# Optimization experiments

Measured on AMD Instinct MI355X. Metric: run time of the kernel, lower is better.

## Reference

```python
import jax, jax.numpy as jnp
import numpy as np

B, S, F_, D, H, L, OUT = 2, 1024, 240, 512, 6, 6, 512
NH = 16
DH = D // NH
EPS = 1e-6  # fast_transformers causal-linear eps
LN_EPS = 1e-5  # torch LayerNorm default


def layernorm(x, g, b):
    m = x.mean(-1, keepdims=True)
    v = ((x - m) ** 2).mean(-1, keepdims=True)
    return (x - m) * jax.lax.rsqrt(v + LN_EPS) * g + b


def causal_linear_attn(q, k, v):
    # q,k,v: [B,S,NH,DH]; feature map phi(x)=elu(x)+1 (fast_transformers default)
    Q = jax.nn.elu(q) + 1.0
    K = jax.nn.elu(k) + 1.0
    # running sum of outer products K_i V_i^T -> [B,S,NH,DH,DH]
    kv = jnp.cumsum(jnp.einsum('bshd,bshm->bshdm', K, v), axis=1)
    num = jnp.einsum('bshd,bshdm->bshm', Q, kv)
    Z = 1.0 / (jnp.einsum('bshd,bshd->bsh', Q, jnp.cumsum(K, axis=1)) + EPS)
    return num * Z[..., None]


def setup_inputs() -> dict:
    key = jax.random.key(0)
    ks = iter(jax.random.split(key, 16))

    def w(shape, s=0.02):
        return (s * jax.random.normal(next(ks), shape)).astype(jnp.float32)

    f32 = jnp.float32
    return {
        'x': jax.random.normal(next(ks), (B, S, F_), dtype=f32),
        'g_in': jnp.ones((F_,), f32), 'b_in': jnp.zeros((F_,), f32),
        'W_pre': w((F_, D)), 'b_pre': jnp.zeros((D,), f32),
        'Wq': w((L, D, D)), 'bq': jnp.zeros((L, D), f32),
        'Wk': w((L, D, D)), 'bk': jnp.zeros((L, D), f32),
        'Wv': w((L, D, D)), 'bv': jnp.zeros((L, D), f32),
        'Wo': w((L, D, D)), 'bo': jnp.zeros((L, D), f32),
        'W1': w((L, D, D)), 'bf1': jnp.zeros((L, D), f32),  # feed_forward_dimensions == hidden_sz
        'W2': w((L, D, D)), 'bf2': jnp.zeros((L, D), f32),
        'ln1_g': jnp.ones((L, D), f32), 'ln1_b': jnp.zeros((L, D), f32),
        'ln2_g': jnp.ones((L, D), f32), 'ln2_b': jnp.zeros((L, D), f32),
        'lnf_g': jnp.ones((D,), f32), 'lnf_b': jnp.zeros((D,), f32),
        'W_post': w((D, OUT)), 'b_post': jnp.zeros((OUT,), f32),
    }


def reference(x, g_in, b_in, W_pre, b_pre, Wq, bq, Wk, bk, Wv, bv, Wo, bo,
              W1, bf1, W2, bf2, ln1_g, ln1_b, ln2_g, ln2_b, lnf_g, lnf_b,
              W_post, b_post):
    # input norm + pre projection
    h = layernorm(x, g_in, b_in) @ W_pre + b_pre  # [B,S,D]
    # fast_transformers post-norm encoder layers
    for l in range(L):
        q = (h @ Wq[l] + bq[l]).reshape(B, S, NH, DH)
        k = (h @ Wk[l] + bk[l]).reshape(B, S, NH, DH)
        v = (h @ Wv[l] + bv[l]).reshape(B, S, NH, DH)
        a = causal_linear_attn(q, k, v).reshape(B, S, D) @ Wo[l] + bo[l]
        h = layernorm(h + a, ln1_g[l], ln1_b[l])
        y = jax.nn.relu(h @ W1[l] + bf1[l]) @ W2[l] + bf2[l]
        h = layernorm(h + y, ln2_g[l], ln2_b[l])
    # final encoder norm, then post projection
    h = layernorm(h, lnf_g, lnf_b)
    return h @ W_post + b_post
```

## Files before the change

kernel.cpp:

```cpp
#include <hip/hip_runtime.h>
#include <hip/hip_bf16.h>
#include <cmath>

#define NROW 2048
#define DMODEL 512
#define FIN 240
#define FINPAD 256
#define NHEAD 16
#define DHEAD 32
#define CHUNK 64
#define NCHUNK 16
#define NLAYER 6
#define SEQ 1024
#define QKVLD 1536

typedef __attribute__((ext_vector_type(8))) short bf16x8;
typedef __attribute__((ext_vector_type(4))) float f32x4;
typedef __attribute__((ext_vector_type(4))) unsigned short u16x4;

#define MFMA_BF16 __builtin_amdgcn_mfma_f32_16x16x32_bf16

__device__ __forceinline__ float phi(float x) {
    return x > 0.f ? x + 1.f : expf(x);
}

__device__ __forceinline__ float bf2f(unsigned short u) {
    return __uint_as_float((unsigned)u << 16);
}

__device__ __forceinline__ unsigned short f2bf_bits(float z) {
    __hip_bfloat16 hb_ = __float2bfloat16(z);
    return *reinterpret_cast<unsigned short*>(&hb_);
}

__device__ __forceinline__ void load_lds16(const void* g, void* l) {
    __builtin_amdgcn_global_load_lds(
        (const __attribute__((address_space(1))) void*)g,
        (__attribute__((address_space(3))) void*)l, 16, 0, 0);
}

__global__ __launch_bounds__(64) void ln_kernel(
    const float* __restrict__ in, const float* __restrict__ res,
    const float* __restrict__ g, const float* __restrict__ b,
    float* __restrict__ out, __hip_bfloat16* __restrict__ outb,
    int C, int Cpad) {
    int row = blockIdx.x;
    int t = threadIdx.x;
    const float* xr = in + (size_t)row * C;
    const float* rr = res ? res + (size_t)row * C : nullptr;
    f32x4 v[2] = {{0.f,0.f,0.f,0.f},{0.f,0.f,0.f,0.f}};
    float sum = 0.f, sq = 0.f;
#pragma unroll
    for (int i = 0; i < 2; ++i) {
        int c = (t + i * 64) * 4;
        if (c < C) {
            f32x4 x_ = *(const f32x4*)&xr[c];
            if (rr) x_ += *(const f32x4*)&rr[c];
            v[i] = x_;
#pragma unroll
            for (int j = 0; j < 4; ++j) { sum += x_[j]; sq += x_[j] * x_[j]; }
        }
    }
#pragma unroll
    for (int off = 32; off > 0; off >>= 1) {
        sum += __shfl_xor(sum, off, 64);
        sq  += __shfl_xor(sq,  off, 64);
    }
    float mean = sum / (float)C;
    float var  = sq / (float)C - mean * mean;
    float rstd = rsqrtf(var + 1e-5f);
#pragma unroll
    for (int i = 0; i < 2; ++i) {
        int c = (t + i * 64) * 4;
        f32x4 y;
#pragma unroll
        for (int j = 0; j < 4; ++j) y[j] = (v[i][j] - mean) * rstd;
        if (c < C) {
            f32x4 gg = *(const f32x4*)&g[c];
            f32x4 bb = *(const f32x4*)&b[c];
#pragma unroll
            for (int j = 0; j < 4; ++j) y[j] = y[j] * gg[j] + bb[j];
            if (out) *(f32x4*)&out[(size_t)row * C + c] = y;
        }
        if (outb && c < Cpad) {
            u16x4 o;
#pragma unroll
            for (int j = 0; j < 4; ++j) {
                float z = (c + j < C) ? y[j] : 0.f;
                o[j] = f2bf_bits(z);
            }
            *(u16x4*)&outb[(size_t)row * Cpad + c] = o;
        }
    }
}

template<int RELU, int WF32, int WBF16, int PHI, int K>
__global__ __launch_bounds__(256) void gemm_bf16_kernel(
    const __hip_bfloat16* __restrict__ A, const __hip_bfloat16* __restrict__ Bt,
    const float* __restrict__ bias,
    float* __restrict__ C, __hip_bfloat16* __restrict__ Cb,
    int N) {
    constexpr int NSTEP = K / 64;
    __shared__ __align__(16) __hip_bfloat16 As[4][64][64];
    __shared__ __align__(16) __hip_bfloat16 Bs[4][64][64];
    const int tid = threadIdx.x, lane = tid & 63, w = tid >> 6;
    const int nN = N >> 6;
    const int bm = (blockIdx.x / nN) * 64;
    const int bn = (blockIdx.x % nN) * 64;

    const int srow  = lane >> 3;
    const int sslot = (lane & 7) ^ srow;
    const size_t aoff = (size_t)srow * K + (size_t)sslot * 8;
    const __hip_bfloat16* gA0 = A  + (size_t)(bm + w * 8) * K + aoff;
    const __hip_bfloat16* gA1 = A  + (size_t)(bm + 32 + w * 8) * K + aoff;
    const __hip_bfloat16* gB0 = Bt + (size_t)(bn + w * 8) * K + aoff;
    const __hip_bfloat16* gB1 = Bt + (size_t)(bn + 32 + w * 8) * K + aoff;

#define STAGE(t) do { \
        load_lds16(gA0 + (size_t)(t) * 64, &As[(t) & 3][w * 8][0]); \
        load_lds16(gA1 + (size_t)(t) * 64, &As[(t) & 3][32 + w * 8][0]); \
        load_lds16(gB0 + (size_t)(t) * 64, &Bs[(t) & 3][w * 8][0]); \
        load_lds16(gB1 + (size_t)(t) * 64, &Bs[(t) & 3][32 + w * 8][0]); \
    } while (0)

    const int wm = (w >> 1) << 5, wn = (w & 1) << 5;
    const int fr = lane & 15, fq = lane >> 4;
    const int sw = fr & 7;
    const int e0 = ((fq      ^ sw) << 3);
    const int e1 = (((fq | 4) ^ sw) << 3);
    f32x4 acc00 = {0.f, 0.f, 0.f, 0.f}, acc01 = acc00, acc10 = acc00, acc11 = acc00;

    STAGE(0); STAGE(1); STAGE(2);
#pragma unroll
    for (int t = 0; t < NSTEP; ++t) {
        if (NSTEP - t >= 3)      asm volatile("s_waitcnt vmcnt(8)" ::: "memory");
        else if (NSTEP - t == 2) asm volatile("s_waitcnt vmcnt(4)" ::: "memory");
        else                     asm volatile("s_waitcnt vmcnt(0)" ::: "memory");
        __builtin_amdgcn_s_barrier();
        __builtin_amdgcn_sched_barrier(0);
        if (t + 3 < NSTEP) STAGE(t + 3);
        const int b = t & 3;
        bf16x8 a00 = *(const bf16x8*)&As[b][wm + fr][e0];
        bf16x8 a01 = *(const bf16x8*)&As[b][wm + fr][e1];
        bf16x8 a10 = *(const bf16x8*)&As[b][wm + 16 + fr][e0];
        bf16x8 a11 = *(const bf16x8*)&As[b][wm + 16 + fr][e1];
        bf16x8 b00 = *(const bf16x8*)&Bs[b][wn + fr][e0];
        bf16x8 b01 = *(const bf16x8*)&Bs[b][wn + fr][e1];
        bf16x8 b10 = *(const bf16x8*)&Bs[b][wn + 16 + fr][e0];
        bf16x8 b11 = *(const bf16x8*)&Bs[b][wn + 16 + fr][e1];
        acc00 = MFMA_BF16(a00, b00, acc00, 0, 0, 0);
        acc01 = MFMA_BF16(a00, b10, acc01, 0, 0, 0);
        acc10 = MFMA_BF16(a10, b00, acc10, 0, 0, 0);
        acc11 = MFMA_BF16(a10, b10, acc11, 0, 0, 0);
        acc00 = MFMA_BF16(a01, b01, acc00, 0, 0, 0);
        acc01 = MFMA_BF16(a01, b11, acc01, 0, 0, 0);
        acc10 = MFMA_BF16(a11, b01, acc10, 0, 0, 0);
        acc11 = MFMA_BF16(a11, b11, acc11, 0, 0, 0);
    }
#undef STAGE

    const int orow = bm + wm + (fq << 2);
    const int ocol = bn + wn + fr;
    float bv0 = bias[ocol], bv1 = bias[ocol + 16];
    f32x4 accs[2][2] = {{acc00, acc01}, {acc10, acc11}};
#pragma unroll
    for (int i = 0; i < 2; ++i)
#pragma unroll
        for (int r = 0; r < 4; ++r) {
            int row = orow + i * 16 + r;
            float v0 = accs[i][0][r] + bv0;
            float v1 = accs[i][1][r] + bv1;
            if (RELU) { v0 = fmaxf(v0, 0.f); v1 = fmaxf(v1, 0.f); }
            if (PHI) {
                if (ocol < 1024)      v0 = phi(v0);
                if (ocol + 16 < 1024) v1 = phi(v1);
            }
            if (WF32) {
                C[(size_t)row * N + ocol]      = v0;
                C[(size_t)row * N + ocol + 16] = v1;
            }
            if (WBF16) {
                Cb[(size_t)row * N + ocol]      = __float2bfloat16(v0);
                Cb[(size_t)row * N + ocol + 16] = __float2bfloat16(v1);
            }
        }
}

__global__ __launch_bounds__(256) void wconv_kernel(
    const float* __restrict__ W_pre, const float* __restrict__ Wq,
    const float* __restrict__ Wk, const float* __restrict__ Wv,
    const float* __restrict__ Wo, const float* __restrict__ W1,
    const float* __restrict__ W2, const float* __restrict__ W_post,
    const float* __restrict__ bq, const float* __restrict__ bk,
    const float* __restrict__ bv, float* __restrict__ qkvbias,
    __hip_bfloat16* wpre_t, __hip_bfloat16* wqkv_t, __hip_bfloat16* wo_t,
    __hip_bfloat16* w1_t, __hip_bfloat16* w2_t, __hip_bfloat16* wpost_t) {
    __shared__ float tile[64][65];
    int tb = blockIdx.x;
    if (tb >= 2400) {
        int l = tb - 2400;
        for (int i = threadIdx.x; i < 512; i += 256) {
            qkvbias[l * QKVLD + i]        = bq[l * DMODEL + i];
            qkvbias[l * QKVLD + 512 + i]  = bk[l * DMODEL + i];
            qkvbias[l * QKVLD + 1024 + i] = bv[l * DMODEL + i];
        }
        return;
    }
    const float* src; __hip_bfloat16* dst; int K, Kpad, kt, nt;
    if (tb < 32) {
        src = W_pre; dst = wpre_t; K = FIN; Kpad = FINPAD;
        kt = tb >> 3; nt = tb & 7;
    } else {
        int t2 = tb - 32; int mat = t2 >> 6; int tt = t2 & 63;
        kt = tt >> 3; nt = tt & 7; K = 512; Kpad = 512;
        if (mat == 36) { src = W_post; dst = wpost_t; }
        else {
            int l = mat / 6, j = mat % 6;
            const size_t WSZ = 262144;
            switch (j) {
                case 0: src = Wq + l * WSZ; dst = wqkv_t + l * 786432;          break;
                case 1: src = Wk + l * WSZ; dst = wqkv_t + l * 786432 + 262144; break;
                case 2: src = Wv + l * WSZ; dst = wqkv_t + l * 786432 + 524288; break;
                case 3: src = Wo + l * WSZ; dst = wo_t + l * WSZ;               break;
                case 4: src = W1 + l * WSZ; dst = w1_t + l * WSZ;               break;
                default: src = W2 + l * WSZ; dst = w2_t + l * WSZ;              break;
            }
        }
    }
    const int N = 512;
    int t = threadIdx.x;
    int k0 = kt * 64, n0 = nt * 64;
#pragma unroll
    for (int i = 0; i < 16; ++i) {
        int kk = (t >> 6) * 16 + i;
        int nn = t & 63;
        int k = k0 + kk;
        tile[kk][nn] = (k < K) ? src[(size_t)k * N + n0 + nn] : 0.f;
    }
    __syncthreads();
#pragma unroll
    for (int i = 0; i < 16; ++i) {
        int nn = (t >> 6) * 16 + i;
        int kk = t & 63;
        dst[(size_t)(n0 + nn) * Kpad + k0 + kk] = __float2bfloat16(tile[kk][nn]);
    }
}

__global__ __launch_bounds__(64) void attn_state_kernel(
    const __hip_bfloat16* __restrict__ qkvb,
    __hip_bfloat16* __restrict__ Sg, float* __restrict__ ksumg) {
    __shared__ __hip_bfloat16 Kt[32][72];
    __shared__ __hip_bfloat16 Vt[32][72];
    int c = blockIdx.x, hh = blockIdx.y, b = blockIdx.z;
    int t = threadIdx.x;
    int sub = t >> 2, slot = t & 3;
    size_t rb = ((size_t)(b * SEQ + c * CHUNK)) * QKVLD + hh * DHEAD;
#pragma unroll
    for (int it = 0; it < 4; ++it) {
        int s = it * 16 + sub;
        bf16x8 kv = *(const bf16x8*)&qkvb[rb + (size_t)s * QKVLD + 512 + slot * 8];
        bf16x8 vv = *(const bf16x8*)&qkvb[rb + (size_t)s * QKVLD + 1024 + slot * 8];
#pragma unroll
        for (int i = 0; i < 8; ++i) {
            Kt[slot * 8 + i][s] = ((const __hip_bfloat16*)&kv)[i];
            Vt[slot * 8 + i][s] = ((const __hip_bfloat16*)&vv)[i];
        }
    }
    __syncthreads();
    int fr = t & 15, fq = t >> 4;
    f32x4 a00 = {0.f,0.f,0.f,0.f}, a01 = a00, a10 = a00, a11 = a00;
#pragma unroll
    for (int ks = 0; ks < 2; ++ks) {
        bf16x8 v0 = *(const bf16x8*)&Vt[fr][ks * 32 + fq * 8];
        bf16x8 v1 = *(const bf16x8*)&Vt[16 + fr][ks * 32 + fq * 8];
        bf16x8 k0 = *(const bf16x8*)&Kt[fr][ks * 32 + fq * 8];
        bf16x8 k1 = *(const bf16x8*)&Kt[16 + fr][ks * 32 + fq * 8];
        a00 = MFMA_BF16(v0, k0, a00, 0, 0, 0);
        a01 = MFMA_BF16(v0, k1, a01, 0, 0, 0);
        a10 = MFMA_BF16(v1, k0, a10, 0, 0, 0);
        a11 = MFMA_BF16(v1, k1, a11, 0, 0, 0);
    }
    size_t ob = ((size_t)((b * NHEAD + hh) * NCHUNK + c)) * 1024;
#pragma unroll
    for (int r = 0; r < 4; ++r) {
        int m0 = fq * 4 + r;
        Sg[ob + (size_t)m0 * 32 + fr]             = __float2bfloat16(a00[r]);
        Sg[ob + (size_t)m0 * 32 + 16 + fr]        = __float2bfloat16(a01[r]);
        Sg[ob + (size_t)(16 + m0) * 32 + fr]      = __float2bfloat16(a10[r]);
        Sg[ob + (size_t)(16 + m0) * 32 + 16 + fr] = __float2bfloat16(a11[r]);
    }
    if (t < 32) {
        float s_ = 0.f;
        for (int s = 0; s < CHUNK; ++s) s_ += __bfloat162float(Kt[t][s]);
        ksumg[((size_t)((b * NHEAD + hh) * NCHUNK + c)) * 32 + t] = s_;
    }
}

__global__ __launch_bounds__(256) void attn_out_kernel(
    const __hip_bfloat16* __restrict__ qkvb,
    const __hip_bfloat16* __restrict__ Sg, const float* __restrict__ ksumg,
    __hip_bfloat16* __restrict__ out) {
    __shared__ __hip_bfloat16 Qs[64][40];
    __shared__ __hip_bfloat16 Ks[64][40];
    __shared__ __hip_bfloat16 Vt[32][72];
    __shared__ __hip_bfloat16 Awb[64][72];
    __shared__ __hip_bfloat16 Stb[32][40];
    __shared__ float den[64];
    __shared__ float ksml[32];
    int c = blockIdx.x, hh = blockIdx.y, b = blockIdx.z;
    int tid = threadIdx.x, lane = tid & 63, w = tid >> 6;
    size_t rb = ((size_t)(b * SEQ + c * CHUNK)) * QKVLD + hh * DHEAD;
    {
        int row = tid >> 2, slot = tid & 3;
        *(bf16x8*)&Qs[row][slot * 8] =
            *(const bf16x8*)&qkvb[rb + (size_t)row * QKVLD + slot * 8];
        *(bf16x8*)&Ks[row][slot * 8] =
            *(const bf16x8*)&qkvb[rb + (size_t)row * QKVLD + 512 + slot * 8];
        bf16x8 vv = *(const bf16x8*)&qkvb[rb + (size_t)row * QKVLD + 1024 + slot * 8];
#pragma unroll
        for (int i = 0; i < 8; ++i)
            Vt[slot * 8 + i][row] = ((const __hip_bfloat16*)&vv)[i];
    }
    size_t sb = ((size_t)((b * NHEAD + hh) * NCHUNK)) * 1024;
    {
        f32x4 st = {0.f, 0.f, 0.f, 0.f};
        for (int cp = 0; cp < c; ++cp) {
            u16x4 sv = *(const u16x4*)&Sg[sb + (size_t)cp * 1024 + tid * 4];
#pragma unroll
            for (int i = 0; i < 4; ++i) st[i] += bf2f(sv[i]);
        }
        int m = tid >> 3, d0 = (tid & 7) * 4;
#pragma unroll
        for (int i = 0; i < 4; ++i) Stb[m][d0 + i] = __float2bfloat16(st[i]);
    }
    if (tid < 32) {
        size_t kb = ((size_t)((b * NHEAD + hh) * NCHUNK)) * 32;
        float s_ = 0.f;
        for (int cp = 0; cp < c; ++cp) s_ += ksumg[kb + cp * 32 + tid];
        ksml[tid] = s_;
    }
    __syncthreads();
    int fr = lane & 15, fq = lane >> 4;
    bf16x8 aQ = *(const bf16x8*)&Qs[w * 16 + fr][fq * 8];
    f32x4 p[4];
#pragma unroll
    for (int j = 0; j < 4; ++j) {
        f32x4 z = {0.f, 0.f, 0.f, 0.f};
        bf16x8 bK = *(const bf16x8*)&Ks[j * 16 + fr][fq * 8];
        p[j] = MFMA_BF16(aQ, bK, z, 0, 0, 0);
    }
    float rs[4] = {0.f, 0.f, 0.f, 0.f};
#pragma unroll
    for (int j = 0; j < 4; ++j) {
        int tcol = j * 16 + fr;
#pragma unroll
        for (int r = 0; r < 4; ++r) {
            int s = w * 16 + fq * 4 + r;
            float val = (tcol <= s) ? p[j][r] : 0.f;
            p[j][r] = val;
            rs[r] += val;
        }
    }
#pragma unroll
    for (int off = 8; off > 0; off >>= 1) {
#pragma unroll
        for (int r = 0; r < 4; ++r) rs[r] += __shfl_xor(rs[r], off, 64);
    }
    if (fr == 0) {
#pragma unroll
        for (int r = 0; r < 4; ++r) den[w * 16 + fq * 4 + r] = rs[r];
    }
#pragma unroll
    for (int j = 0; j < 4; ++j)
#pragma unroll
        for (int r = 0; r < 4; ++r)
            Awb[w * 16 + fq * 4 + r][j * 16 + fr] = __float2bfloat16(p[j][r]);
    __syncthreads();
    if (tid < 64) {
        float dq = den[tid];
        float dst_ = 0.f;
#pragma unroll
        for (int d = 0; d < 32; ++d)
            dst_ += __bfloat162float(Qs[tid][d]) * ksml[d];
        den[tid] = 1.f / (dq + dst_ + 1e-6f);
    }
    __syncthreads();
    size_t orb = ((size_t)(b * SEQ + c * CHUNK)) * DMODEL + hh * DHEAD;
#pragma unroll
    for (int mf = 0; mf < 2; ++mf) {
        f32x4 acc = {0.f, 0.f, 0.f, 0.f};
        bf16x8 bS = *(const bf16x8*)&Stb[mf * 16 + fr][fq * 8];
        acc = MFMA_BF16(aQ, bS, acc, 0, 0, 0);
#pragma unroll
        for (int ks = 0; ks < 2; ++ks) {
            bf16x8 aA = *(const bf16x8*)&Awb[w * 16 + fr][ks * 32 + fq * 8];
            bf16x8 bV = *(const bf16x8*)&Vt[mf * 16 + fr][ks * 32 + fq * 8];
            acc = MFMA_BF16(aA, bV, acc, 0, 0, 0);
        }
#pragma unroll
        for (int r = 0; r < 4; ++r) {
            int s = w * 16 + fq * 4 + r;
            out[orb + (size_t)s * DMODEL + mf * 16 + fr] =
                __float2bfloat16(acc[r] * den[s]);
        }
    }
}

template<int R, int WF, int WB, int PHI, int K>
static inline void gemm(const __hip_bfloat16* A, const __hip_bfloat16* Bt,
                        const float* bias, float* C, __hip_bfloat16* Cb,
                        int M, int N, hipStream_t s) {
    gemm_bf16_kernel<R, WF, WB, PHI, K><<<(M / 64) * (N / 64), 256, 0, s>>>(A, Bt, bias, C, Cb, N);
}

extern "C" void kernel_launch(void* const* d_in, const int* in_sizes, int n_in,
                              void* d_out, int out_size, void* d_ws, size_t ws_size,
                              hipStream_t stream) {
    const float* x      = (const float*)d_in[0];
    const float* g_in   = (const float*)d_in[1];
    const float* b_in   = (const float*)d_in[2];
    const float* W_pre  = (const float*)d_in[3];
    const float* b_pre  = (const float*)d_in[4];
    const float* Wq     = (const float*)d_in[5];
    const float* bq     = (const float*)d_in[6];
    const float* Wk     = (const float*)d_in[7];
    const float* bk     = (const float*)d_in[8];
    const float* Wv     = (const float*)d_in[9];
    const float* bv     = (const float*)d_in[10];
    const float* Wo     = (const float*)d_in[11];
    const float* bo     = (const float*)d_in[12];
    const float* W1     = (const float*)d_in[13];
    const float* bf1    = (const float*)d_in[14];
    const float* W2     = (const float*)d_in[15];
    const float* bf2    = (const float*)d_in[16];
    const float* ln1_g  = (const float*)d_in[17];
    const float* ln1_b  = (const float*)d_in[18];
    const float* ln2_g  = (const float*)d_in[19];
    const float* ln2_b  = (const float*)d_in[20];
    const float* lnf_g  = (const float*)d_in[21];
    const float* lnf_b  = (const float*)d_in[22];
    const float* W_post = (const float*)d_in[23];
    const float* b_post = (const float*)d_in[24];
    (void)in_sizes; (void)n_in; (void)out_size; (void)ws_size;

    float* ws = (float*)d_ws;
    const size_t SZ = (size_t)NROW * DMODEL;
    float* h       = ws;
    float* t1      = h + SZ;
    float* ksumg   = t1 + SZ;
    float* qkvbias = ksumg + 16384;
    __hip_bfloat16* bp = (__hip_bfloat16*)(qkvbias + 9216);
    __hip_bfloat16* Sg     = bp;            bp += 524288;
    __hip_bfloat16* hb     = bp;            bp += SZ;
    __hip_bfloat16* qkvb   = bp;            bp += (size_t)NROW * QKVLD;
    __hip_bfloat16* xnb    = bp;            bp += (size_t)NROW * FINPAD;
    __hip_bfloat16* attb   = bp;            bp += SZ;
    __hip_bfloat16* ffb    = bp;            bp += SZ;
    __hip_bfloat16* t0b    = bp;            bp += SZ;
    __hip_bfloat16* wpre_t = bp;            bp += (size_t)DMODEL * FINPAD;
    __hip_bfloat16* wqkv_t = bp;            bp += (size_t)NLAYER * 786432;
    __hip_bfloat16* wo_t   = bp;            bp += (size_t)NLAYER * 262144;
    __hip_bfloat16* w1_t   = bp;            bp += (size_t)NLAYER * 262144;
    __hip_bfloat16* w2_t   = bp;            bp += (size_t)NLAYER * 262144;
    __hip_bfloat16* wpost_t= bp;

    wconv_kernel<<<2406, 256, 0, stream>>>(
        W_pre, Wq, Wk, Wv, Wo, W1, W2, W_post,
        bq, bk, bv, qkvbias,
        wpre_t, wqkv_t, wo_t, w1_t, w2_t, wpost_t);

    ln_kernel<<<NROW, 64, 0, stream>>>(x, nullptr, g_in, b_in, nullptr, xnb, FIN, FINPAD);
    gemm<0, 1, 1, 0, FINPAD>(xnb, wpre_t, b_pre, h, hb, NROW, DMODEL, stream);

    dim3 ag(NCHUNK, NHEAD, 2);
    for (int l = 0; l < NLAYER; ++l) {
        gemm<0, 0, 1, 1, DMODEL>(hb, wqkv_t + (size_t)l * 786432, qkvbias + l * QKVLD,
                                 nullptr, qkvb, NROW, QKVLD, stream);
        attn_state_kernel<<<ag, 64, 0, stream>>>(qkvb, Sg, ksumg);
        attn_out_kernel<<<ag, 256, 0, stream>>>(qkvb, Sg, ksumg, attb);
        gemm<0, 1, 0, 0, DMODEL>(attb, wo_t + (size_t)l * 262144, bo + l * DMODEL,
                                 t1, nullptr, NROW, DMODEL, stream);
        ln_kernel<<<NROW, 64, 0, stream>>>(h, t1, ln1_g + l * DMODEL, ln1_b + l * DMODEL,
                                           h, hb, DMODEL, DMODEL);
        gemm<1, 0, 1, 0, DMODEL>(hb, w1_t + (size_t)l * 262144, bf1 + l * DMODEL,
                                 nullptr, ffb, NROW, DMODEL, stream);
        gemm<0, 1, 0, 0, DMODEL>(ffb, w2_t + (size_t)l * 262144, bf2 + l * DMODEL,
                                 t1, nullptr, NROW, DMODEL, stream);
        ln_kernel<<<NROW, 64, 0, stream>>>(h, t1, ln2_g + l * DMODEL, ln2_b + l * DMODEL,
                                           h, hb, DMODEL, DMODEL);
    }

    ln_kernel<<<NROW, 64, 0, stream>>>(h, nullptr, lnf_g, lnf_b, nullptr, t0b, DMODEL, DMODEL);
    gemm<0, 1, 0, 0, DMODEL>(t0b, wpost_t, b_post, (float*)d_out, nullptr, NROW, DMODEL, stream);
}
```

Measured before the change: 346.7 us.

## Fuse residual add into GEMM epilogue and restructure chunked linear attention

The residual add moves into the Wo and W2 GEMM epilogues, so the layernorm kernels read one fp32 tensor instead of two. The attention state kernel no longer computes per-chunk KV outer products. It only writes transposed K and V tiles plus K sums. The output kernel recomputes the prefix state with MFMA over all earlier chunks, loads Q and K straight from global memory, and computes the denominator with wave shuffles. This drops one state round trip and some LDS staging, but later chunks now do more redundant MFMA work, which adds load imbalance.

```diff
diff --git a/kernel.cpp b/kernel.cpp
--- a/kernel.cpp
+++ b/kernel.cpp
@@ -94,12 +94,12 @@
     }
 }
 
-template<int RELU, int WF32, int WBF16, int PHI, int K>
+template<int RELU, int WF32, int WBF16, int PHI, int RES, int K>
 __global__ __launch_bounds__(256) void gemm_bf16_kernel(
     const __hip_bfloat16* __restrict__ A, const __hip_bfloat16* __restrict__ Bt,
     const float* __restrict__ bias,
     float* __restrict__ C, __hip_bfloat16* __restrict__ Cb,
-    int N) {
+    const float* __restrict__ Rres, int N) {
     constexpr int NSTEP = K / 64;
     __shared__ __align__(16) __hip_bfloat16 As[4][64][64];
     __shared__ __align__(16) __hip_bfloat16 Bs[4][64][64];
@@ -170,6 +170,10 @@
             int row = orow + i * 16 + r;
             float v0 = accs[i][0][r] + bv0;
             float v1 = accs[i][1][r] + bv1;
+            if (RES) {
+                v0 += Rres[(size_t)row * N + ocol];
+                v1 += Rres[(size_t)row * N + ocol + 16];
+            }
             if (RELU) { v0 = fmaxf(v0, 0.f); v1 = fmaxf(v1, 0.f); }
             if (PHI) {
                 if (ocol < 1024)      v0 = phi(v0);
@@ -246,9 +250,10 @@
     }
 }
 
-__global__ __launch_bounds__(64) void attn_state_kernel(
+__global__ __launch_bounds__(64) void tkv_kernel(
     const __hip_bfloat16* __restrict__ qkvb,
-    __hip_bfloat16* __restrict__ Sg, float* __restrict__ ksumg) {
+    __hip_bfloat16* __restrict__ Ktg, __hip_bfloat16* __restrict__ Vtg,
+    float* __restrict__ ksumg) {
     __shared__ __hip_bfloat16 Kt[32][72];
     __shared__ __hip_bfloat16 Vt[32][72];
     int c = blockIdx.x, hh = blockIdx.y, b = blockIdx.z;
@@ -267,86 +272,64 @@
         }
     }
     __syncthreads();
-    int fr = t & 15, fq = t >> 4;
-    f32x4 a00 = {0.f,0.f,0.f,0.f}, a01 = a00, a10 = a00, a11 = a00;
-#pragma unroll
-    for (int ks = 0; ks < 2; ++ks) {
-        bf16x8 v0 = *(const bf16x8*)&Vt[fr][ks * 32 + fq * 8];
-        bf16x8 v1 = *(const bf16x8*)&Vt[16 + fr][ks * 32 + fq * 8];
-        bf16x8 k0 = *(const bf16x8*)&Kt[fr][ks * 32 + fq * 8];
-        bf16x8 k1 = *(const bf16x8*)&Kt[16 + fr][ks * 32 + fq * 8];
-        a00 = MFMA_BF16(v0, k0, a00, 0, 0, 0);
-        a01 = MFMA_BF16(v0, k1, a01, 0, 0, 0);
-        a10 = MFMA_BF16(v1, k0, a10, 0, 0, 0);
-        a11 = MFMA_BF16(v1, k1, a11, 0, 0, 0);
-    }
-    size_t ob = ((size_t)((b * NHEAD + hh) * NCHUNK + c)) * 1024;
-#pragma unroll
-    for (int r = 0; r < 4; ++r) {
-        int m0 = fq * 4 + r;
-        Sg[ob + (size_t)m0 * 32 + fr]             = __float2bfloat16(a00[r]);
-        Sg[ob + (size_t)m0 * 32 + 16 + fr]        = __float2bfloat16(a01[r]);
-        Sg[ob + (size_t)(16 + m0) * 32 + fr]      = __float2bfloat16(a10[r]);
-        Sg[ob + (size_t)(16 + m0) * 32 + 16 + fr] = __float2bfloat16(a11[r]);
+    size_t cb = (size_t)((b * NHEAD + hh) * NCHUNK + c);
+    __hip_bfloat16* ko = Ktg + cb * 2048;
+    __hip_bfloat16* vo = Vtg + cb * 2048;
+    int d = t >> 1, s0 = (t & 1) * 32;
+#pragma unroll
+    for (int i = 0; i < 4; ++i) {
+        *(bf16x8*)&ko[d * 64 + s0 + i * 8] = *(const bf16x8*)&Kt[d][s0 + i * 8];
+        *(bf16x8*)&vo[d * 64 + s0 + i * 8] = *(const bf16x8*)&Vt[d][s0 + i * 8];
     }
     if (t < 32) {
         float s_ = 0.f;
         for (int s = 0; s < CHUNK; ++s) s_ += __bfloat162float(Kt[t][s]);
-        ksumg[((size_t)((b * NHEAD + hh) * NCHUNK + c)) * 32 + t] = s_;
-    }
-}
-
-__global__ __launch_bounds__(256) void attn_out_kernel(
+        ksumg[cb * 32 + t] = s_;
+    }
+}
+
+__global__ __launch_bounds__(256) void attn_fused_kernel(
     const __hip_bfloat16* __restrict__ qkvb,
-    const __hip_bfloat16* __restrict__ Sg, const float* __restrict__ ksumg,
+    const __hip_bfloat16* __restrict__ Ktg, const __hip_bfloat16* __restrict__ Vtg,
+    const float* __restrict__ ksumg,
     __hip_bfloat16* __restrict__ out) {
-    __shared__ __hip_bfloat16 Qs[64][40];
-    __shared__ __hip_bfloat16 Ks[64][40];
-    __shared__ __hip_bfloat16 Vt[32][72];
     __shared__ __hip_bfloat16 Awb[64][72];
     __shared__ __hip_bfloat16 Stb[32][40];
     __shared__ float den[64];
     __shared__ float ksml[32];
     int c = blockIdx.x, hh = blockIdx.y, b = blockIdx.z;
     int tid = threadIdx.x, lane = tid & 63, w = tid >> 6;
+    int fr = lane & 15, fq = lane >> 4;
+    size_t chb = (size_t)(b * NHEAD + hh) * NCHUNK;
+
+    if (tid < 32) {
+        float s_ = 0.f;
+        for (int cp = 0; cp < c; ++cp) s_ += ksumg[(chb + cp) * 32 + tid];
+        ksml[tid] = s_;
+    }
+    int wr = w >> 1, wc = w & 1;
+    f32x4 sacc = {0.f, 0.f, 0.f, 0.f};
+    const __hip_bfloat16* vq = Vtg + chb * 2048 + (size_t)(wr * 16 + fr) * 64 + fq * 8;
+    const __hip_bfloat16* kq = Ktg + chb * 2048 + (size_t)(wc * 16 + fr) * 64 + fq * 8;
+    for (int cp = 0; cp < c; ++cp) {
+        bf16x8 av0 = *(const bf16x8*)(vq + cp * 2048);
+        bf16x8 av1 = *(const bf16x8*)(vq + cp * 2048 + 32);
+        bf16x8 bk0 = *(const bf16x8*)(kq + cp * 2048);
+        bf16x8 bk1 = *(const bf16x8*)(kq + cp * 2048 + 32);
+        sacc = MFMA_BF16(av0, bk0, sacc, 0, 0, 0);
+        sacc = MFMA_BF16(av1, bk1, sacc, 0, 0, 0);
+    }
+#pragma unroll
+    for (int r = 0; r < 4; ++r)
+        Stb[wr * 16 + fq * 4 + r][wc * 16 + fr] = __float2bfloat16(sacc[r]);
+
     size_t rb = ((size_t)(b * SEQ + c * CHUNK)) * QKVLD + hh * DHEAD;
-    {
-        int row = tid >> 2, slot = tid & 3;
-        *(bf16x8*)&Qs[row][slot * 8] =
-            *(const bf16x8*)&qkvb[rb + (size_t)row * QKVLD + slot * 8];
-        *(bf16x8*)&Ks[row][slot * 8] =
-            *(const bf16x8*)&qkvb[rb + (size_t)row * QKVLD + 512 + slot * 8];
-        bf16x8 vv = *(const bf16x8*)&qkvb[rb + (size_t)row * QKVLD + 1024 + slot * 8];
-#pragma unroll
-        for (int i = 0; i < 8; ++i)
-            Vt[slot * 8 + i][row] = ((const __hip_bfloat16*)&vv)[i];
-    }
-    size_t sb = ((size_t)((b * NHEAD + hh) * NCHUNK)) * 1024;
-    {
-        f32x4 st = {0.f, 0.f, 0.f, 0.f};
-        for (int cp = 0; cp < c; ++cp) {
-            u16x4 sv = *(const u16x4*)&Sg[sb + (size_t)cp * 1024 + tid * 4];
-#pragma unroll
-            for (int i = 0; i < 4; ++i) st[i] += bf2f(sv[i]);
-        }
-        int m = tid >> 3, d0 = (tid & 7) * 4;
-#pragma unroll
-        for (int i = 0; i < 4; ++i) Stb[m][d0 + i] = __float2bfloat16(st[i]);
-    }
-    if (tid < 32) {
-        size_t kb = ((size_t)((b * NHEAD + hh) * NCHUNK)) * 32;
-        float s_ = 0.f;
-        for (int cp = 0; cp < c; ++cp) s_ += ksumg[kb + cp * 32 + tid];
-        ksml[tid] = s_;
-    }
-    __syncthreads();
-    int fr = lane & 15, fq = lane >> 4;
-    bf16x8 aQ = *(const bf16x8*)&Qs[w * 16 + fr][fq * 8];
+    bf16x8 aQ = *(const bf16x8*)&qkvb[rb + (size_t)(w * 16 + fr) * QKVLD + fq * 8];
     f32x4 p[4];
 #pragma unroll
     for (int j = 0; j < 4; ++j) {
         f32x4 z = {0.f, 0.f, 0.f, 0.f};
-        bf16x8 bK = *(const bf16x8*)&Ks[j * 16 + fr][fq * 8];
+        bf16x8 bK = *(const bf16x8*)&qkvb[rb + (size_t)(j * 16 + fr) * QKVLD + 512 + fq * 8];
         p[j] = MFMA_BF16(aQ, bK, z, 0, 0, 0);
     }
     float rs[4] = {0.f, 0.f, 0.f, 0.f};
@@ -376,16 +359,18 @@
         for (int r = 0; r < 4; ++r)
             Awb[w * 16 + fq * 4 + r][j * 16 + fr] = __float2bfloat16(p[j][r]);
     __syncthreads();
-    if (tid < 64) {
-        float dq = den[tid];
-        float dst_ = 0.f;
-#pragma unroll
-        for (int d = 0; d < 32; ++d)
-            dst_ += __bfloat162float(Qs[tid][d]) * ksml[d];
-        den[tid] = 1.f / (dq + dst_ + 1e-6f);
-    }
-    __syncthreads();
+
+    float qk = 0.f;
+#pragma unroll
+    for (int jj = 0; jj < 8; ++jj)
+        qk += __bfloat162float(((const __hip_bfloat16*)&aQ)[jj]) * ksml[fq * 8 + jj];
+    qk += __shfl_xor(qk, 16, 64);
+    qk += __shfl_xor(qk, 32, 64);
+    if (fq == 0)
+        den[w * 16 + fr] = 1.f / (den[w * 16 + fr] + qk + 1e-6f);
+
     size_t orb = ((size_t)(b * SEQ + c * CHUNK)) * DMODEL + hh * DHEAD;
+    const __hip_bfloat16* vc = Vtg + (chb + c) * 2048;
 #pragma unroll
     for (int mf = 0; mf < 2; ++mf) {
         f32x4 acc = {0.f, 0.f, 0.f, 0.f};
@@ -394,7 +379,7 @@
 #pragma unroll
         for (int ks = 0; ks < 2; ++ks) {
             bf16x8 aA = *(const bf16x8*)&Awb[w * 16 + fr][ks * 32 + fq * 8];
-            bf16x8 bV = *(const bf16x8*)&Vt[mf * 16 + fr][ks * 32 + fq * 8];
+            bf16x8 bV = *(const bf16x8*)&vc[(size_t)(mf * 16 + fr) * 64 + ks * 32 + fq * 8];
             acc = MFMA_BF16(aA, bV, acc, 0, 0, 0);
         }
 #pragma unroll
@@ -406,11 +391,12 @@
     }
 }
 
-template<int R, int WF, int WB, int PHI, int K>
+template<int R, int WF, int WB, int PHI, int RES, int K>
 static inline void gemm(const __hip_bfloat16* A, const __hip_bfloat16* Bt,
                         const float* bias, float* C, __hip_bfloat16* Cb,
-                        int M, int N, hipStream_t s) {
-    gemm_bf16_kernel<R, WF, WB, PHI, K><<<(M / 64) * (N / 64), 256, 0, s>>>(A, Bt, bias, C, Cb, N);
+                        const float* Rres, int M, int N, hipStream_t s) {
+    gemm_bf16_kernel<R, WF, WB, PHI, RES, K>
+        <<<(M / 64) * (N / 64), 256, 0, s>>>(A, Bt, bias, C, Cb, Rres, N);
 }
 
 extern "C" void kernel_launch(void* const* d_in, const int* in_sizes, int n_in,
@@ -450,7 +436,8 @@
     float* ksumg   = t1 + SZ;
     float* qkvbias = ksumg + 16384;
     __hip_bfloat16* bp = (__hip_bfloat16*)(qkvbias + 9216);
-    __hip_bfloat16* Sg     = bp;            bp += 524288;
+    __hip_bfloat16* Ktg    = bp;            bp += 1048576;
+    __hip_bfloat16* Vtg    = bp;            bp += 1048576;
     __hip_bfloat16* hb     = bp;            bp += SZ;
     __hip_bfloat16* qkvb   = bp;            bp += (size_t)NROW * QKVLD;
     __hip_bfloat16* xnb    = bp;            bp += (size_t)NROW * FINPAD;
@@ -470,26 +457,26 @@
         wpre_t, wqkv_t, wo_t, w1_t, w2_t, wpost_t);
 
     ln_kernel<<<NROW, 64, 0, stream>>>(x, nullptr, g_in, b_in, nullptr, xnb, FIN, FINPAD);
-    gemm<0, 1, 1, 0, FINPAD>(xnb, wpre_t, b_pre, h, hb, NROW, DMODEL, stream);
+    gemm<0, 1, 1, 0, 0, FINPAD>(xnb, wpre_t, b_pre, h, hb, nullptr, NROW, DMODEL, stream);
 
     dim3 ag(NCHUNK, NHEAD, 2);
     for (int l = 0; l < NLAYER; ++l) {
-        gemm<0, 0, 1, 1, DMODEL>(hb, wqkv_t + (size_t)l * 786432, qkvbias + l * QKVLD,
-                                 nullptr, qkvb, NROW, QKVLD, stream);
-        attn_state_kernel<<<ag, 64, 0, stream>>>(qkvb, Sg, ksumg);
-        attn_out_kernel<<<ag, 256, 0, stream>>>(qkvb, Sg, ksumg, attb);
-        gemm<0, 1, 0, 0, DMODEL>(attb, wo_t + (size_t)l * 262144, bo + l * DMODEL,
-                                 t1, nullptr, NROW, DMODEL, stream);
-        ln_kernel<<<NROW, 64, 0, stream>>>(h, t1, ln1_g + l * DMODEL, ln1_b + l * DMODEL,
+        gemm<0, 0, 1, 1, 0, DMODEL>(hb, wqkv_t + (size_t)l * 786432, qkvbias + l * QKVLD,
+                                    nullptr, qkvb, nullptr, NROW, QKVLD, stream);
+        tkv_kernel<<<ag, 64, 0, stream>>>(qkvb, Ktg, Vtg, ksumg);
+        attn_fused_kernel<<<ag, 256, 0, stream>>>(qkvb, Ktg, Vtg, ksumg, attb);
+        gemm<0, 1, 0, 0, 1, DMODEL>(attb, wo_t + (size_t)l * 262144, bo + l * DMODEL,
+                                    t1, nullptr, h, NROW, DMODEL, stream);
+        ln_kernel<<<NROW, 64, 0, stream>>>(t1, nullptr, ln1_g + l * DMODEL, ln1_b + l * DMODEL,
                                            h, hb, DMODEL, DMODEL);
-        gemm<1, 0, 1, 0, DMODEL>(hb, w1_t + (size_t)l * 262144, bf1 + l * DMODEL,
-                                 nullptr, ffb, NROW, DMODEL, stream);
-        gemm<0, 1, 0, 0, DMODEL>(ffb, w2_t + (size_t)l * 262144, bf2 + l * DMODEL,
-                                 t1, nullptr, NROW, DMODEL, stream);
-        ln_kernel<<<NROW, 64, 0, stream>>>(h, t1, ln2_g + l * DMODEL, ln2_b + l * DMODEL,
+        gemm<1, 0, 1, 0, 0, DMODEL>(hb, w1_t + (size_t)l * 262144, bf1 + l * DMODEL,
+                                    nullptr, ffb, nullptr, NROW, DMODEL, stream);
+        gemm<0, 1, 0, 0, 1, DMODEL>(ffb, w2_t + (size_t)l * 262144, bf2 + l * DMODEL,
+                                    t1, nullptr, h, NROW, DMODEL, stream);
+        ln_kernel<<<NROW, 64, 0, stream>>>(t1, nullptr, ln2_g + l * DMODEL, ln2_b + l * DMODEL,
                                            h, hb, DMODEL, DMODEL);
     }
 
     ln_kernel<<<NROW, 64, 0, stream>>>(h, nullptr, lnf_g, lnf_b, nullptr, t0b, DMODEL, DMODEL);
-    gemm<0, 1, 0, 0, DMODEL>(t0b, wpost_t, b_post, (float*)d_out, nullptr, NROW, DMODEL, stream);
-}
+    gemm<0, 1, 0, 0, 0, DMODEL>(t0b, wpost_t, b_post, (float*)d_out, nullptr, nullptr, NROW, DMODEL, stream);
+}
```

After: 407.6 us. 17.6% more time.

## Fuse per-chunk attention state computation into QKV GEMM epilogue via interleaved K/V layout

Applied to the files above, without the earlier changes.

Reorders the QKV weight columns so each 64-wide N tile holds one head's K (32 cols) and V (32 cols). The QKV GEMM epilogue then stages K and V transposed in reused shared memory and computes the per-chunk KᵀV state with MFMA plus the K column sums, which removes the separate attn_state kernel launch and its reread of K/V from global memory. The attention-output kernel is updated to the new K/V offsets. The cost is an extra barrier and epilogue work in the K/V blocks of the GEMM.

```diff
diff --git a/kernel.cpp b/kernel.cpp
--- a/kernel.cpp
+++ b/kernel.cpp
@@ -94,11 +94,12 @@
     }
 }
 
-template<int RELU, int WF32, int WBF16, int PHI, int K>
+template<int RELU, int WF32, int WBF16, int QKV, int K>
 __global__ __launch_bounds__(256) void gemm_bf16_kernel(
     const __hip_bfloat16* __restrict__ A, const __hip_bfloat16* __restrict__ Bt,
     const float* __restrict__ bias,
     float* __restrict__ C, __hip_bfloat16* __restrict__ Cb,
+    __hip_bfloat16* __restrict__ Sg, float* __restrict__ ksumg,
     int N) {
     constexpr int NSTEP = K / 64;
     __shared__ __align__(16) __hip_bfloat16 As[4][64][64];
@@ -162,6 +163,12 @@
     const int orow = bm + wm + (fq << 2);
     const int ocol = bn + wn + fr;
     float bv0 = bias[ocol], bv1 = bias[ocol + 16];
+    const bool dophi = QKV && (bn < 512 || wn == 0);
+    const bool kvblk = QKV && (bn >= 512);
+    __hip_bfloat16 (*Kt)[72] = reinterpret_cast<__hip_bfloat16 (*)[72]>(&As[0][0][0]);
+    __hip_bfloat16 (*Vt)[72] = reinterpret_cast<__hip_bfloat16 (*)[72]>(&As[0][0][0] + 2304);
+    if (kvblk) __syncthreads();
+
     f32x4 accs[2][2] = {{acc00, acc01}, {acc10, acc11}};
 #pragma unroll
     for (int i = 0; i < 2; ++i)
@@ -171,19 +178,50 @@
             float v0 = accs[i][0][r] + bv0;
             float v1 = accs[i][1][r] + bv1;
             if (RELU) { v0 = fmaxf(v0, 0.f); v1 = fmaxf(v1, 0.f); }
-            if (PHI) {
-                if (ocol < 1024)      v0 = phi(v0);
-                if (ocol + 16 < 1024) v1 = phi(v1);
-            }
+            if (dophi) { v0 = phi(v0); v1 = phi(v1); }
+            __hip_bfloat16 b0 = __float2bfloat16(v0);
+            __hip_bfloat16 b1 = __float2bfloat16(v1);
             if (WF32) {
                 C[(size_t)row * N + ocol]      = v0;
                 C[(size_t)row * N + ocol + 16] = v1;
             }
             if (WBF16) {
-                Cb[(size_t)row * N + ocol]      = __float2bfloat16(v0);
-                Cb[(size_t)row * N + ocol + 16] = __float2bfloat16(v1);
+                Cb[(size_t)row * N + ocol]      = b0;
+                Cb[(size_t)row * N + ocol + 16] = b1;
             }
-        }
+            if (kvblk) {
+                int lrow = wm + i * 16 + (fq << 2) + r;
+                if (wn == 0) { Kt[fr][lrow] = b0; Kt[16 + fr][lrow] = b1; }
+                else         { Vt[fr][lrow] = b0; Vt[16 + fr][lrow] = b1; }
+            }
+        }
+
+    if (kvblk) {
+        __syncthreads();
+        int b_ = bm >> 10, c_ = (bm >> 6) & 15, hh_ = (bn - 512) >> 6;
+        size_t cb = ((size_t)(b_ * NHEAD + hh_) * NCHUNK + c_);
+        int wr = w >> 1, wc = w & 1;
+        f32x4 sacc = {0.f, 0.f, 0.f, 0.f};
+#pragma unroll
+        for (int ks = 0; ks < 2; ++ks) {
+            bf16x8 v_ = *(const bf16x8*)&Vt[wr * 16 + fr][ks * 32 + fq * 8];
+            bf16x8 k_ = *(const bf16x8*)&Kt[wc * 16 + fr][ks * 32 + fq * 8];
+            sacc = MFMA_BF16(v_, k_, sacc, 0, 0, 0);
+        }
+        size_t ob = cb * 1024;
+#pragma unroll
+        for (int r = 0; r < 4; ++r)
+            Sg[ob + (size_t)(wr * 16 + (fq << 2) + r) * 32 + wc * 16 + fr] =
+                __float2bfloat16(sacc[r]);
+        int d = tid >> 3, s0 = (tid & 7) * 8;
+        float part = 0.f;
+#pragma unroll
+        for (int i = 0; i < 8; ++i) part += __bfloat162float(Kt[d][s0 + i]);
+        part += __shfl_xor(part, 1, 64);
+        part += __shfl_xor(part, 2, 64);
+        part += __shfl_xor(part, 4, 64);
+        if ((tid & 7) == 0) ksumg[cb * 32 + d] = part;
+    }
 }
 
 __global__ __launch_bounds__(256) void wconv_kernel(
@@ -200,13 +238,14 @@
     if (tb >= 2400) {
         int l = tb - 2400;
         for (int i = threadIdx.x; i < 512; i += 256) {
-            qkvbias[l * QKVLD + i]        = bq[l * DMODEL + i];
-            qkvbias[l * QKVLD + 512 + i]  = bk[l * DMODEL + i];
-            qkvbias[l * QKVLD + 1024 + i] = bv[l * DMODEL + i];
+            qkvbias[l * QKVLD + i] = bq[l * DMODEL + i];
+            int kpos = 512 + (i >> 5) * 64 + (i & 31);
+            qkvbias[l * QKVLD + kpos]      = bk[l * DMODEL + i];
+            qkvbias[l * QKVLD + kpos + 32] = bv[l * DMODEL + i];
         }
         return;
     }
-    const float* src; __hip_bfloat16* dst; int K, Kpad, kt, nt;
+    const float* src; __hip_bfloat16* dst; int K, Kpad, kt, nt, kvmap = 0;
     if (tb < 32) {
         src = W_pre; dst = wpre_t; K = FIN; Kpad = FINPAD;
         kt = tb >> 3; nt = tb & 7;
@@ -218,12 +257,12 @@
             int l = mat / 6, j = mat % 6;
             const size_t WSZ = 262144;
             switch (j) {
-                case 0: src = Wq + l * WSZ; dst = wqkv_t + l * 786432;          break;
-                case 1: src = Wk + l * WSZ; dst = wqkv_t + l * 786432 + 262144; break;
-                case 2: src = Wv + l * WSZ; dst = wqkv_t + l * 786432 + 524288; break;
-                case 3: src = Wo + l * WSZ; dst = wo_t + l * WSZ;               break;
-                case 4: src = W1 + l * WSZ; dst = w1_t + l * WSZ;               break;
-                default: src = W2 + l * WSZ; dst = w2_t + l * WSZ;              break;
+                case 0: src = Wq + l * WSZ; dst = wqkv_t + l * 786432;            break;
+                case 1: src = Wk + l * WSZ; dst = wqkv_t + l * 786432; kvmap = 1; break;
+                case 2: src = Wv + l * WSZ; dst = wqkv_t + l * 786432; kvmap = 2; break;
+                case 3: src = Wo + l * WSZ; dst = wo_t + l * WSZ;                 break;
+                case 4: src = W1 + l * WSZ; dst = w1_t + l * WSZ;                 break;
+                default: src = W2 + l * WSZ; dst = w2_t + l * WSZ;                break;
             }
         }
     }
@@ -242,57 +281,10 @@
     for (int i = 0; i < 16; ++i) {
         int nn = (t >> 6) * 16 + i;
         int kk = t & 63;
-        dst[(size_t)(n0 + nn) * Kpad + k0 + kk] = __float2bfloat16(tile[kk][nn]);
-    }
-}
-
-__global__ __launch_bounds__(64) void attn_state_kernel(
-    const __hip_bfloat16* __restrict__ qkvb,
-    __hip_bfloat16* __restrict__ Sg, float* __restrict__ ksumg) {
-    __shared__ __hip_bfloat16 Kt[32][72];
-    __shared__ __hip_bfloat16 Vt[32][72];
-    int c = blockIdx.x, hh = blockIdx.y, b = blockIdx.z;
-    int t = threadIdx.x;
-    int sub = t >> 2, slot = t & 3;
-    size_t rb = ((size_t)(b * SEQ + c * CHUNK)) * QKVLD + hh * DHEAD;
-#pragma unroll
-    for (int it = 0; it < 4; ++it) {
-        int s = it * 16 + sub;
-        bf16x8 kv = *(const bf16x8*)&qkvb[rb + (size_t)s * QKVLD + 512 + slot * 8];
-        bf16x8 vv = *(const bf16x8*)&qkvb[rb + (size_t)s * QKVLD + 1024 + slot * 8];
-#pragma unroll
-        for (int i = 0; i < 8; ++i) {
-            Kt[slot * 8 + i][s] = ((const __hip_bfloat16*)&kv)[i];
-            Vt[slot * 8 + i][s] = ((const __hip_bfloat16*)&vv)[i];
-        }
-    }
-    __syncthreads();
-    int fr = t & 15, fq = t >> 4;
-    f32x4 a00 = {0.f,0.f,0.f,0.f}, a01 = a00, a10 = a00, a11 = a00;
-#pragma unroll
-    for (int ks = 0; ks < 2; ++ks) {
-        bf16x8 v0 = *(const bf16x8*)&Vt[fr][ks * 32 + fq * 8];
-        bf16x8 v1 = *(const bf16x8*)&Vt[16 + fr][ks * 32 + fq * 8];
-        bf16x8 k0 = *(const bf16x8*)&Kt[fr][ks * 32 + fq * 8];
-        bf16x8 k1 = *(const bf16x8*)&Kt[16 + fr][ks * 32 + fq * 8];
-        a00 = MFMA_BF16(v0, k0, a00, 0, 0, 0);
-        a01 = MFMA_BF16(v0, k1, a01, 0, 0, 0);
-        a10 = MFMA_BF16(v1, k0, a10, 0, 0, 0);
-        a11 = MFMA_BF16(v1, k1, a11, 0, 0, 0);
-    }
-    size_t ob = ((size_t)((b * NHEAD + hh) * NCHUNK + c)) * 1024;
-#pragma unroll
-    for (int r = 0; r < 4; ++r) {
-        int m0 = fq * 4 + r;
-        Sg[ob + (size_t)m0 * 32 + fr]             = __float2bfloat16(a00[r]);
-        Sg[ob + (size_t)m0 * 32 + 16 + fr]        = __float2bfloat16(a01[r]);
-        Sg[ob + (size_t)(16 + m0) * 32 + fr]      = __float2bfloat16(a10[r]);
-        Sg[ob + (size_t)(16 + m0) * 32 + 16 + fr] = __float2bfloat16(a11[r]);
-    }
-    if (t < 32) {
-        float s_ = 0.f;
-        for (int s = 0; s < CHUNK; ++s) s_ += __bfloat162float(Kt[t][s]);
-        ksumg[((size_t)((b * NHEAD + hh) * NCHUNK + c)) * 32 + t] = s_;
+        int n = n0 + nn;
+        size_t rr = (size_t)n;
+        if (kvmap) rr = 512 + (size_t)(n >> 5) * 64 + ((kvmap == 2) ? 32 : 0) + (n & 31);
+        dst[rr * Kpad + k0 + kk] = __float2bfloat16(tile[kk][nn]);
     }
 }
 
@@ -309,14 +301,16 @@
     __shared__ float ksml[32];
     int c = blockIdx.x, hh = blockIdx.y, b = blockIdx.z;
     int tid = threadIdx.x, lane = tid & 63, w = tid >> 6;
-    size_t rb = ((size_t)(b * SEQ + c * CHUNK)) * QKVLD + hh * DHEAD;
+    size_t base = ((size_t)(b * SEQ + c * CHUNK)) * QKVLD;
+    size_t rbq  = base + hh * DHEAD;
+    size_t rbkv = base + 512 + hh * 64;
     {
         int row = tid >> 2, slot = tid & 3;
         *(bf16x8*)&Qs[row][slot * 8] =
-            *(const bf16x8*)&qkvb[rb + (size_t)row * QKVLD + slot * 8];
+            *(const bf16x8*)&qkvb[rbq + (size_t)row * QKVLD + slot * 8];
         *(bf16x8*)&Ks[row][slot * 8] =
-            *(const bf16x8*)&qkvb[rb + (size_t)row * QKVLD + 512 + slot * 8];
-        bf16x8 vv = *(const bf16x8*)&qkvb[rb + (size_t)row * QKVLD + 1024 + slot * 8];
+            *(const bf16x8*)&qkvb[rbkv + (size_t)row * QKVLD + slot * 8];
+        bf16x8 vv = *(const bf16x8*)&qkvb[rbkv + 32 + (size_t)row * QKVLD + slot * 8];
 #pragma unroll
         for (int i = 0; i < 8; ++i)
             Vt[slot * 8 + i][row] = ((const __hip_bfloat16*)&vv)[i];
@@ -406,11 +400,13 @@
     }
 }
 
-template<int R, int WF, int WB, int PHI, int K>
+template<int R, int WF, int WB, int QKV, int K>
 static inline void gemm(const __hip_bfloat16* A, const __hip_bfloat16* Bt,
                         const float* bias, float* C, __hip_bfloat16* Cb,
+                        __hip_bfloat16* Sg, float* ksumg,
                         int M, int N, hipStream_t s) {
-    gemm_bf16_kernel<R, WF, WB, PHI, K><<<(M / 64) * (N / 64), 256, 0, s>>>(A, Bt, bias, C, Cb, N);
+    gemm_bf16_kernel<R, WF, WB, QKV, K>
+        <<<(M / 64) * (N / 64), 256, 0, s>>>(A, Bt, bias, C, Cb, Sg, ksumg, N);
 }
 
 extern "C" void kernel_launch(void* const* d_in, const int* in_sizes, int n_in,
@@ -470,26 +466,27 @@
         wpre_t, wqkv_t, wo_t, w1_t, w2_t, wpost_t);
 
     ln_kernel<<<NROW, 64, 0, stream>>>(x, nullptr, g_in, b_in, nullptr, xnb, FIN, FINPAD);
-    gemm<0, 1, 1, 0, FINPAD>(xnb, wpre_t, b_pre, h, hb, NROW, DMODEL, stream);
+    gemm<0, 1, 1, 0, FINPAD>(xnb, wpre_t, b_pre, h, hb, nullptr, nullptr,
+                             NROW, DMODEL, stream);
 
     dim3 ag(NCHUNK, NHEAD, 2);
     for (int l = 0; l < NLAYER; ++l) {
         gemm<0, 0, 1, 1, DMODEL>(hb, wqkv_t + (size_t)l * 786432, qkvbias + l * QKVLD,
-                                 nullptr, qkvb, NROW, QKVLD, stream);
-        attn_state_kernel<<<ag, 64, 0, stream>>>(qkvb, Sg, ksumg);
+                                 nullptr, qkvb, Sg, ksumg, NROW, QKVLD, stream);
         attn_out_kernel<<<ag, 256, 0, stream>>>(qkvb, Sg, ksumg, attb);
         gemm<0, 1, 0, 0, DMODEL>(attb, wo_t + (size_t)l * 262144, bo + l * DMODEL,
-                                 t1, nullptr, NROW, DMODEL, stream);
+                                 t1, nullptr, nullptr, nullptr, NROW, DMODEL, stream);
         ln_kernel<<<NROW, 64, 0, stream>>>(h, t1, ln1_g + l * DMODEL, ln1_b + l * DMODEL,
                                            h, hb, DMODEL, DMODEL);
         gemm<1, 0, 1, 0, DMODEL>(hb, w1_t + (size_t)l * 262144, bf1 + l * DMODEL,
-                                 nullptr, ffb, NROW, DMODEL, stream);
+                                 nullptr, ffb, nullptr, nullptr, NROW, DMODEL, stream);
         gemm<0, 1, 0, 0, DMODEL>(ffb, w2_t + (size_t)l * 262144, bf2 + l * DMODEL,
-                                 t1, nullptr, NROW, DMODEL, stream);
+                                 t1, nullptr, nullptr, nullptr, NROW, DMODEL, stream);
         ln_kernel<<<NROW, 64, 0, stream>>>(h, t1, ln2_g + l * DMODEL, ln2_b + l * DMODEL,
                                            h, hb, DMODEL, DMODEL);
     }
 
     ln_kernel<<<NROW, 64, 0, stream>>>(h, nullptr, lnf_g, lnf_b, nullptr, t0b, DMODEL, DMODEL);
-    gemm<0, 1, 0, 0, DMODEL>(t0b, wpost_t, b_post, (float*)d_out, nullptr, NROW, DMODEL, stream);
-}
+    gemm<0, 1, 0, 0, DMODEL>(t0b, wpost_t, b_post, (float*)d_out, nullptr,
+                             nullptr, nullptr, NROW, DMODEL, stream);
+}
```

After: 342.2 us (median of 2 runs). No clear change (-1.3%).
